# Kernel tuning notes

Measured on AMD Instinct MI355X. Metric: run time of the kernel, lower is better.

The kernel has to match this reference:

```python
import jax, jax.numpy as jnp
import numpy as np

D_MODEL = 768
NUM_HEADS = 12
DIM_QKV = D_MODEL // NUM_HEADS  # 64
NEG_INF = -1000000000.0


def setup_inputs() -> dict:
    key = jax.random.key(0)
    ks = jax.random.split(key, 12)
    B, S = 2, 2048
    def lin(kw, kb):
        # torch nn.Linear default init: U(-1/sqrt(fan_in), 1/sqrt(fan_in))
        bound = 1.0 / np.sqrt(D_MODEL)
        W = jax.random.uniform(kw, (D_MODEL, D_MODEL), jnp.float32, -bound, bound)
        b = jax.random.uniform(kb, (D_MODEL,), jnp.float32, -bound, bound)
        return W, b
    Wq, bq = lin(ks[0], ks[1])
    Wk, bk = lin(ks[2], ks[3])
    Wv, bv = lin(ks[4], ks[5])
    Wo, bo = lin(ks[6], ks[7])
    Q = jax.random.normal(ks[8], (B, S, D_MODEL), jnp.float32)
    K = jax.random.normal(ks[9], (B, S, D_MODEL), jnp.float32)
    V = jax.random.normal(ks[10], (B, S, D_MODEL), jnp.float32)
    mask = jnp.tril(jnp.ones((S, S), dtype=bool))[None, None]  # [1,1,S,S] causal
    return {"Q": Q, "K": K, "V": V, "mask": mask,
            "Wq": Wq, "bq": bq, "Wk": Wk, "bk": bk,
            "Wv": Wv, "bv": bv, "Wo": Wo, "bo": bo}


def _split_heads(x):
    B, S, _ = x.shape
    return x.reshape(B, S, NUM_HEADS, DIM_QKV).transpose(0, 2, 1, 3)  # [B,H,S,d]


def reference(Q, K, V, mask, Wq, bq, Wk, bk, Wv, bv, Wo, bo):
    # torch Linear: y = x @ W.T + b
    q = _split_heads(Q @ Wq.T + bq)
    k = _split_heads(K @ Wk.T + bk)
    v = _split_heads(V @ Wv.T + bv)
    scale = jnp.sqrt(jnp.float32(DIM_QKV))
    scores = jnp.einsum('bhqd,bhkd->bhqk', q, k) / scale  # [B,H,S,S]
    scores = jnp.where(mask, scores, NEG_INF)
    probs = jax.nn.softmax(scores, axis=-1)  # dropout p=0 -> identity
    attn = jnp.einsum('bhqk,bhkd->bhqd', probs, v)
    B, H, S, d = attn.shape
    out = attn.transpose(0, 2, 1, 3).reshape(B, S, H * d) @ Wo.T + bo
    return out, scores
```

## Files before the change

### kernel.cpp

```cpp
#include <hip/hip_runtime.h>
#include <hip/hip_bf16.h>

typedef __attribute__((ext_vector_type(8))) short short8;
typedef __attribute__((ext_vector_type(4))) short short4v;
typedef __attribute__((ext_vector_type(4))) float f32x4;

#define S_LEN 2048
#define DM 768
#define NH 12
#define HD 64
#define NB 2
#define MROWS (NB*S_LEN)
#define NEGINF (-1.0e9f)
#define XEL 3145728
#define WEL 589824

__device__ __forceinline__ unsigned short f2bf(float x) {
    __hip_bfloat16 h = __float2bfloat16(x);
    return *reinterpret_cast<unsigned short*>(&h);
}

__device__ __forceinline__ void gl_lds16(const unsigned short* g, unsigned short* l) {
    __builtin_amdgcn_global_load_lds(
        (const __attribute__((address_space(1))) unsigned int*)g,
        (__attribute__((address_space(3))) unsigned int*)l, 16, 0, 0);
}

__global__ __launch_bounds__(256) void cvt_w_kernel(
    const float* w0, const float* w1, const float* w2, const float* w3,
    unsigned short* dst)
{
    int which = blockIdx.y;
    const float* src = (which == 0) ? w0 : (which == 1) ? w1 : (which == 2) ? w2 : w3;
    size_t idx = (size_t)blockIdx.x * 256 + threadIdx.x;
    const float* s = src + idx * 8;
    f32x4 v0 = *(const f32x4*)s;
    f32x4 v1 = *(const f32x4*)(s + 4);
    short8 o;
    o[0] = (short)f2bf(v0[0]); o[1] = (short)f2bf(v0[1]);
    o[2] = (short)f2bf(v0[2]); o[3] = (short)f2bf(v0[3]);
    o[4] = (short)f2bf(v1[0]); o[5] = (short)f2bf(v1[1]);
    o[6] = (short)f2bf(v1[2]); o[7] = (short)f2bf(v1[3]);
    *(short8*)&dst[(size_t)which * WEL + idx * 8] = o;
}

__global__ __launch_bounds__(256) void gemm_qkv_kernel(
    const float* Xq, const float* Xk, const float* Xv, const unsigned short* Wall,
    const float* b0, const float* b1, const float* b2, unsigned short* qh)
{
    int by = blockIdx.y;
    const float* A = (by == 0) ? Xq : (by == 1) ? Xk : Xv;
    const unsigned short* W = Wall + (size_t)by * WEL;
    const float* bias = (by == 0) ? b0 : (by == 1) ? b1 : b2;
    int bx = blockIdx.x;
    int im = (bx & 7) + 8 * (bx / 48);
    int jn = (bx >> 3) % 6;
    int i0 = im * 128, j0 = jn * 128;

    __shared__ unsigned short As[128 * 64];
    __shared__ unsigned short Ws[128 * 64];

    int t = threadIdx.x;
    int w = t >> 6, lane = t & 63, g = lane >> 4, fr = lane & 15;
    int wm = w >> 1, wn = w & 1;

    f32x4 acc[4][4];
    for (int i = 0; i < 4; ++i)
        for (int j = 0; j < 4; ++j)
            acc[i][j] = (f32x4){0.f, 0.f, 0.f, 0.f};

    int boff = t * 16;
    int arow = t >> 3;
    int acol = (t & 7) * 8;

    for (int k0 = 0; k0 < DM; k0 += 64) {
        __syncthreads();
        for (int r = 0; r < 4; ++r) {
            int b = r * 4096 + boff;
            int row = b >> 7, colb = b & 127;
            gl_lds16(&W[(size_t)(j0 + row) * DM + k0 + (colb >> 1)],
                     (unsigned short*)((char*)Ws + b));
        }
        for (int rr = 0; rr < 4; ++rr) {
            int row = rr * 32 + arow;
            const float* src = &A[(size_t)(i0 + row) * DM + k0 + acol];
            f32x4 v0 = *(const f32x4*)src;
            f32x4 v1 = *(const f32x4*)(src + 4);
            short8 o;
            o[0] = (short)f2bf(v0[0]); o[1] = (short)f2bf(v0[1]);
            o[2] = (short)f2bf(v0[2]); o[3] = (short)f2bf(v0[3]);
            o[4] = (short)f2bf(v1[0]); o[5] = (short)f2bf(v1[1]);
            o[6] = (short)f2bf(v1[2]); o[7] = (short)f2bf(v1[3]);
            *(short8*)&As[row * 64 + acol] = o;
        }
        __syncthreads();
        for (int kk = 0; kk < 2; ++kk) {
            short8 af[4], wf[4];
            for (int it = 0; it < 4; ++it)
                af[it] = *(const short8*)&As[(wm * 64 + it * 16 + fr) * 64 + kk * 32 + g * 8];
            for (int jt = 0; jt < 4; ++jt)
                wf[jt] = *(const short8*)&Ws[(wn * 64 + jt * 16 + fr) * 64 + kk * 32 + g * 8];
            for (int it = 0; it < 4; ++it)
                for (int jt = 0; jt < 4; ++jt)
                    acc[it][jt] = __builtin_amdgcn_mfma_f32_16x16x32_bf16(af[it], wf[jt], acc[it][jt], 0, 0, 0);
        }
    }

    float scl = (by == 0) ? 0.125f : 1.0f;
    if (by < 2) {
        unsigned short* outp = qh + (size_t)by * XEL;
        for (int jt = 0; jt < 4; ++jt) {
            int j = j0 + wn * 64 + jt * 16 + fr;
            float bv = bias[j];
            int h = j >> 6, dq = j & 63;
            for (int it = 0; it < 4; ++it)
                for (int r = 0; r < 4; ++r) {
                    int i = i0 + wm * 64 + it * 16 + g * 4 + r;
                    int bb = i >> 11, s = i & 2047;
                    outp[((size_t)((bb * NH + h) * S_LEN) + s) * HD + dq] = f2bf((acc[it][jt][r] + bv) * scl);
                }
        }
    } else {
        unsigned short* vtp = qh + (size_t)2 * XEL;
        for (int jt = 0; jt < 4; ++jt) {
            int j = j0 + wn * 64 + jt * 16 + fr;
            float bv = bias[j];
            int h = j >> 6, dq = j & 63;
            for (int it = 0; it < 4; ++it) {
                int ibase = i0 + wm * 64 + it * 16 + g * 4;
                int bb = ibase >> 11, s = ibase & 2047;
                short4v o;
                for (int r = 0; r < 4; ++r) o[r] = (short)f2bf(acc[it][jt][r] + bv);
                *(short4v*)&vtp[((size_t)(bb * NH + h) * HD + dq) * S_LEN + s] = o;
            }
        }
    }
}

__global__ __launch_bounds__(256) void gemm_o_kernel(
    const unsigned short* A, const unsigned short* W, const float* bias, float* f_out)
{
    int bx = blockIdx.x;
    int im = (bx & 7) + 8 * (bx / 96);
    int jn = (bx >> 3) % 12;
    int i0 = im * 64, j0 = jn * 64;

    __shared__ unsigned short As[64 * 64];
    __shared__ unsigned short Ws[64 * 64];

    int t = threadIdx.x;
    int w = t >> 6, lane = t & 63, g = lane >> 4, fr = lane & 15;
    int wm = w >> 1, wn = w & 1;

    f32x4 acc[2][2];
    for (int i = 0; i < 2; ++i)
        for (int j = 0; j < 2; ++j)
            acc[i][j] = (f32x4){0.f, 0.f, 0.f, 0.f};

    int boff = t * 16;

    for (int k0 = 0; k0 < DM; k0 += 64) {
        __syncthreads();
        for (int r = 0; r < 2; ++r) {
            int b = r * 4096 + boff;
            int row = b >> 7, colb = b & 127;
            gl_lds16(&A[(size_t)(i0 + row) * DM + k0 + (colb >> 1)],
                     (unsigned short*)((char*)As + b));
            gl_lds16(&W[(size_t)(j0 + row) * DM + k0 + (colb >> 1)],
                     (unsigned short*)((char*)Ws + b));
        }
        __syncthreads();
        for (int kk = 0; kk < 2; ++kk) {
            short8 af[2], wf[2];
            for (int it = 0; it < 2; ++it)
                af[it] = *(const short8*)&As[(wm * 32 + it * 16 + fr) * 64 + kk * 32 + g * 8];
            for (int jt = 0; jt < 2; ++jt)
                wf[jt] = *(const short8*)&Ws[(wn * 32 + jt * 16 + fr) * 64 + kk * 32 + g * 8];
            for (int it = 0; it < 2; ++it)
                for (int jt = 0; jt < 2; ++jt)
                    acc[it][jt] = __builtin_amdgcn_mfma_f32_16x16x32_bf16(af[it], wf[jt], acc[it][jt], 0, 0, 0);
        }
    }

    for (int jt = 0; jt < 2; ++jt) {
        int j = j0 + wn * 32 + jt * 16 + fr;
        float bv = bias[j];
        for (int it = 0; it < 2; ++it)
            for (int r = 0; r < 4; ++r) {
                int i = i0 + wm * 32 + it * 16 + g * 4 + r;
                f_out[(size_t)i * DM + j] = acc[it][jt][r] + bv;
            }
    }
}

__global__ __launch_bounds__(256) void attn_kernel(
    const unsigned short* q, const unsigned short* k, const unsigned short* vt,
    float* scores, unsigned short* attn)
{
    __shared__ unsigned short KV[2][8192];
    __shared__ float P[4][16][68];
    int t = threadIdx.x;
    int w = t >> 6, lane = t & 63, g = lane >> 4, fr = lane & 15;
    float (*Pw)[68] = P[w];

    int bid = blockIdx.x;
    int bh = (bid & 7) * 3 + (bid >> 3) % 3;
    int s = bid / 24;
    int myspan = (w < 2) ? s : 63 - s;
    int qbase = myspan * 32 + (w & 1) * 16;
    int myNt = ((myspan * 32 + 31) >> 6) + 1;
    int ntmax = (((63 - s) * 32 + 31) >> 6) + 1;
    int b = bh / NH, h = bh % NH;

    const unsigned short* qp = q + (size_t)bh * S_LEN * HD;
    const unsigned short* kp = k + (size_t)bh * S_LEN * HD;
    const unsigned short* vp = vt + (size_t)bh * HD * S_LEN;
    float* sp = scores + (size_t)bh * S_LEN * S_LEN;

    int srow2 = t >> 3;
    int scb = (t & 7) * 16;
    int swzu = (fr & 7) * 8;

    short8 qf0 = *(const short8*)&qp[(size_t)(qbase + fr) * HD + g * 8];
    short8 qf1 = *(const short8*)&qp[(size_t)(qbase + fr) * HD + 32 + g * 8];

    f32x4 acc[4];
    for (int jt = 0; jt < 4; ++jt) acc[jt] = (f32x4){0.f, 0.f, 0.f, 0.f};
    float m_run = -1e30f, l_run = 0.f;

    for (int rd = 0; rd < 2; ++rd) {
        int row = rd * 32 + srow2;
        int sc = (scb ^ ((row & 7) << 4)) >> 1;
        gl_lds16(&kp[(size_t)row * HD + sc], &KV[0][(size_t)t * 8 + rd * 2048]);
        gl_lds16(&vp[(size_t)row * S_LEN + sc], &KV[0][4096 + (size_t)t * 8 + rd * 2048]);
    }

    int buf = 0;
    for (int kt = 0; kt < ntmax; ++kt) {
        __syncthreads();
        if (kt + 1 < ntmax) {
            int kb2 = (kt + 1) * 64;
            for (int rd = 0; rd < 2; ++rd) {
                int row = rd * 32 + srow2;
                int sc = (scb ^ ((row & 7) << 4)) >> 1;
                gl_lds16(&kp[(size_t)(kb2 + row) * HD + sc], &KV[buf ^ 1][(size_t)t * 8 + rd * 2048]);
                gl_lds16(&vp[(size_t)row * S_LEN + kb2 + sc], &KV[buf ^ 1][4096 + (size_t)t * 8 + rd * 2048]);
            }
        }
        if (kt < myNt) {
            const unsigned short* Kb = KV[buf];
            const unsigned short* Vb = KV[buf] + 4096;
            int kb = kt * 64;
            bool diag = (kt == myNt - 1);

            short8 kf[4][2];
            for (int ktt = 0; ktt < 4; ++ktt) {
                int base = (ktt * 16 + fr) * 64;
                kf[ktt][0] = *(const short8*)&Kb[base + ((g * 8) ^ swzu)];
                kf[ktt][1] = *(const short8*)&Kb[base + ((32 + g * 8) ^ swzu)];
            }
            __builtin_amdgcn_s_setprio(1);
            f32x4 s4v[4];
            for (int ktt = 0; ktt < 4; ++ktt) {
                f32x4 s4 = (f32x4){0.f, 0.f, 0.f, 0.f};
                s4 = __builtin_amdgcn_mfma_f32_16x16x32_bf16(qf0, kf[ktt][0], s4, 0, 0, 0);
                s4 = __builtin_amdgcn_mfma_f32_16x16x32_bf16(qf1, kf[ktt][1], s4, 0, 0, 0);
                s4v[ktt] = s4;
            }
            __builtin_amdgcn_s_setprio(0);
            if (diag) {
                for (int ktt = 0; ktt < 4; ++ktt) {
                    int kg = kb + ktt * 16 + fr;
                    for (int r = 0; r < 4; ++r) {
                        int qg = qbase + g * 4 + r;
                        float val = (kg <= qg) ? s4v[ktt][r] : NEGINF;
                        Pw[g * 4 + r][ktt * 16 + fr] = val;
                    }
                }
            } else {
                for (int ktt = 0; ktt < 4; ++ktt)
                    for (int r = 0; r < 4; ++r)
                        Pw[g * 4 + r][ktt * 16 + fr] = s4v[ktt][r];
            }
            for (int pass = 0; pass < 4; ++pass) {
                int rr = pass * 4 + g;
                int cc = fr * 4;
                f32x4 vv = *(const f32x4*)&Pw[rr][cc];
                __builtin_nontemporal_store(vv, (f32x4*)&sp[(size_t)(qbase + rr) * S_LEN + kb + cc]);
            }
            f32x4 pA = *(const f32x4*)&Pw[fr][g * 8];
            f32x4 pB = *(const f32x4*)&Pw[fr][g * 8 + 4];
            f32x4 pC = *(const f32x4*)&Pw[fr][32 + g * 8];
            f32x4 pD = *(const f32x4*)&Pw[fr][32 + g * 8 + 4];
            float pv[16];
            pv[0]=pA[0]; pv[1]=pA[1]; pv[2]=pA[2]; pv[3]=pA[3];
            pv[4]=pB[0]; pv[5]=pB[1]; pv[6]=pB[2]; pv[7]=pB[3];
            pv[8]=pC[0]; pv[9]=pC[1]; pv[10]=pC[2]; pv[11]=pC[3];
            pv[12]=pD[0]; pv[13]=pD[1]; pv[14]=pD[2]; pv[15]=pD[3];
            float tmax = pv[0];
            for (int e = 1; e < 16; ++e) tmax = fmaxf(tmax, pv[e]);
            tmax = fmaxf(tmax, __shfl_xor(tmax, 16, 64));
            tmax = fmaxf(tmax, __shfl_xor(tmax, 32, 64));
            float m_new = fmaxf(m_run, tmax);
            float corr = __expf(m_run - m_new);
            float lsum = 0.f;
            for (int e = 0; e < 16; ++e) { pv[e] = __expf(pv[e] - m_new); lsum += pv[e]; }
            lsum += __shfl_xor(lsum, 16, 64);
            lsum += __shfl_xor(lsum, 32, 64);
            l_run = l_run * corr + lsum;
            m_run = m_new;
            short8 pa0, pa1;
            for (int e = 0; e < 8; ++e) { pa0[e] = (short)f2bf(pv[e]); pa1[e] = (short)f2bf(pv[8 + e]); }
            float fc[4];
            for (int r = 0; r < 4; ++r) fc[r] = __shfl(corr, g * 4 + r, 64);
            for (int jt = 0; jt < 4; ++jt)
                for (int r = 0; r < 4; ++r) acc[jt][r] *= fc[r];
            short8 vf[4][2];
            for (int jt = 0; jt < 4; ++jt) {
                int base = (jt * 16 + fr) * 64;
                vf[jt][0] = *(const short8*)&Vb[base + ((g * 8) ^ swzu)];
                vf[jt][1] = *(const short8*)&Vb[base + ((32 + g * 8) ^ swzu)];
            }
            __builtin_amdgcn_s_setprio(1);
            for (int jt = 0; jt < 4; ++jt) {
                acc[jt] = __builtin_amdgcn_mfma_f32_16x16x32_bf16(pa0, vf[jt][0], acc[jt], 0, 0, 0);
                acc[jt] = __builtin_amdgcn_mfma_f32_16x16x32_bf16(pa1, vf[jt][1], acc[jt], 0, 0, 0);
            }
            __builtin_amdgcn_s_setprio(0);
        }
        buf ^= 1;
    }
    float linv[4];
    for (int r = 0; r < 4; ++r) linv[r] = 1.0f / __shfl(l_run, g * 4 + r, 64);
    for (int jt = 0; jt < 4; ++jt) {
        int col = h * HD + jt * 16 + fr;
        for (int r = 0; r < 4; ++r) {
            int i = b * S_LEN + qbase + g * 4 + r;
            attn[(size_t)i * DM + col] = f2bf(acc[jt][r] * linv[r]);
        }
    }
    f32x4 nv = (f32x4){NEGINF, NEGINF, NEGINF, NEGINF};
    int fill0 = myNt * 64;
    for (int rr = 0; rr < 16; ++rr) {
        float* rowp = &sp[(size_t)(qbase + rr) * S_LEN];
        for (int c = fill0 + lane * 4; c < S_LEN; c += 256)
            __builtin_nontemporal_store(nv, (f32x4*)(rowp + c));
    }
}

extern "C" void kernel_launch(void* const* d_in, const int* in_sizes, int n_in,
                              void* d_out, int out_size, void* d_ws, size_t ws_size,
                              hipStream_t stream) {
    const float* Q  = (const float*)d_in[0];
    const float* K  = (const float*)d_in[1];
    const float* V  = (const float*)d_in[2];
    const float* Wq = (const float*)d_in[4];
    const float* bq = (const float*)d_in[5];
    const float* Wk = (const float*)d_in[6];
    const float* bk = (const float*)d_in[7];
    const float* Wv = (const float*)d_in[8];
    const float* bv = (const float*)d_in[9];
    const float* Wo = (const float*)d_in[10];
    const float* bo = (const float*)d_in[11];

    float* out = (float*)d_out;
    float* scores = out + (size_t)MROWS * DM;

    unsigned short* ws   = (unsigned short*)d_ws;
    unsigned short* Wbf  = ws;
    unsigned short* qh   = Wbf + (size_t)4 * WEL;
    unsigned short* attn = qh + (size_t)3 * XEL;

    cvt_w_kernel<<<dim3(288, 4), 256, 0, stream>>>(Wq, Wk, Wv, Wo, Wbf);
    gemm_qkv_kernel<<<dim3(192, 3), 256, 0, stream>>>(Q, K, V, Wbf, bq, bk, bv, qh);
    attn_kernel<<<dim3(768), 256, 0, stream>>>(qh, qh + (size_t)XEL, qh + (size_t)2 * XEL,
                                               scores, attn);
    gemm_o_kernel<<<dim3(768), 256, 0, stream>>>(attn, Wbf + (size_t)3 * WEL, bo, out);
}
```

Baseline: 157.5 us.

## Load K/V fragments directly from global memory instead of LDS double buffer

New measurement: 175.7 us. 11.5% more time.

```diff
diff --git a/kernel.cpp b/kernel.cpp
--- a/kernel.cpp
+++ b/kernel.cpp
@@ -197,7 +197,6 @@
     const unsigned short* q, const unsigned short* k, const unsigned short* vt,
     float* scores, unsigned short* attn)
 {
-    __shared__ unsigned short KV[2][8192];
     __shared__ float P[4][16][68];
     int t = threadIdx.x;
     int w = t >> 6, lane = t & 63, g = lane >> 4, fr = lane & 15;
@@ -209,7 +208,6 @@
     int myspan = (w < 2) ? s : 63 - s;
     int qbase = myspan * 32 + (w & 1) * 16;
     int myNt = ((myspan * 32 + 31) >> 6) + 1;
-    int ntmax = (((63 - s) * 32 + 31) >> 6) + 1;
     int b = bh / NH, h = bh % NH;
 
     const unsigned short* qp = q + (size_t)bh * S_LEN * HD;
@@ -217,10 +215,6 @@
     const unsigned short* vp = vt + (size_t)bh * HD * S_LEN;
     float* sp = scores + (size_t)bh * S_LEN * S_LEN;
 
-    int srow2 = t >> 3;
-    int scb = (t & 7) * 16;
-    int swzu = (fr & 7) * 8;
-
     short8 qf0 = *(const short8*)&qp[(size_t)(qbase + fr) * HD + g * 8];
     short8 qf1 = *(const short8*)&qp[(size_t)(qbase + fr) * HD + 32 + g * 8];
 
@@ -228,107 +222,82 @@
     for (int jt = 0; jt < 4; ++jt) acc[jt] = (f32x4){0.f, 0.f, 0.f, 0.f};
     float m_run = -1e30f, l_run = 0.f;
 
-    for (int rd = 0; rd < 2; ++rd) {
-        int row = rd * 32 + srow2;
-        int sc = (scb ^ ((row & 7) << 4)) >> 1;
-        gl_lds16(&kp[(size_t)row * HD + sc], &KV[0][(size_t)t * 8 + rd * 2048]);
-        gl_lds16(&vp[(size_t)row * S_LEN + sc], &KV[0][4096 + (size_t)t * 8 + rd * 2048]);
-    }
-
-    int buf = 0;
-    for (int kt = 0; kt < ntmax; ++kt) {
-        __syncthreads();
-        if (kt + 1 < ntmax) {
-            int kb2 = (kt + 1) * 64;
-            for (int rd = 0; rd < 2; ++rd) {
-                int row = rd * 32 + srow2;
-                int sc = (scb ^ ((row & 7) << 4)) >> 1;
-                gl_lds16(&kp[(size_t)(kb2 + row) * HD + sc], &KV[buf ^ 1][(size_t)t * 8 + rd * 2048]);
-                gl_lds16(&vp[(size_t)row * S_LEN + kb2 + sc], &KV[buf ^ 1][4096 + (size_t)t * 8 + rd * 2048]);
+    for (int kt = 0; kt < myNt; ++kt) {
+        int kb = kt * 64;
+        bool diag = (kt == myNt - 1);
+
+        short8 kf[4][2];
+        for (int ktt = 0; ktt < 4; ++ktt) {
+            kf[ktt][0] = *(const short8*)&kp[(size_t)(kb + ktt * 16 + fr) * HD + g * 8];
+            kf[ktt][1] = *(const short8*)&kp[(size_t)(kb + ktt * 16 + fr) * HD + 32 + g * 8];
+        }
+        __builtin_amdgcn_s_setprio(1);
+        f32x4 s4v[4];
+        for (int ktt = 0; ktt < 4; ++ktt) {
+            f32x4 s4 = (f32x4){0.f, 0.f, 0.f, 0.f};
+            s4 = __builtin_amdgcn_mfma_f32_16x16x32_bf16(qf0, kf[ktt][0], s4, 0, 0, 0);
+            s4 = __builtin_amdgcn_mfma_f32_16x16x32_bf16(qf1, kf[ktt][1], s4, 0, 0, 0);
+            s4v[ktt] = s4;
+        }
+        __builtin_amdgcn_s_setprio(0);
+        if (diag) {
+            for (int ktt = 0; ktt < 4; ++ktt) {
+                int kg = kb + ktt * 16 + fr;
+                for (int r = 0; r < 4; ++r) {
+                    int qg = qbase + g * 4 + r;
+                    float val = (kg <= qg) ? s4v[ktt][r] : NEGINF;
+                    Pw[g * 4 + r][ktt * 16 + fr] = val;
+                }
             }
-        }
-        if (kt < myNt) {
-            const unsigned short* Kb = KV[buf];
-            const unsigned short* Vb = KV[buf] + 4096;
-            int kb = kt * 64;
-            bool diag = (kt == myNt - 1);
-
-            short8 kf[4][2];
-            for (int ktt = 0; ktt < 4; ++ktt) {
-                int base = (ktt * 16 + fr) * 64;
-                kf[ktt][0] = *(const short8*)&Kb[base + ((g * 8) ^ swzu)];
-                kf[ktt][1] = *(const short8*)&Kb[base + ((32 + g * 8) ^ swzu)];
-            }
-            __builtin_amdgcn_s_setprio(1);
-            f32x4 s4v[4];
-            for (int ktt = 0; ktt < 4; ++ktt) {
-                f32x4 s4 = (f32x4){0.f, 0.f, 0.f, 0.f};
-                s4 = __builtin_amdgcn_mfma_f32_16x16x32_bf16(qf0, kf[ktt][0], s4, 0, 0, 0);
-                s4 = __builtin_amdgcn_mfma_f32_16x16x32_bf16(qf1, kf[ktt][1], s4, 0, 0, 0);
-                s4v[ktt] = s4;
-            }
-            __builtin_amdgcn_s_setprio(0);
-            if (diag) {
-                for (int ktt = 0; ktt < 4; ++ktt) {
-                    int kg = kb + ktt * 16 + fr;
-                    for (int r = 0; r < 4; ++r) {
-                        int qg = qbase + g * 4 + r;
-                        float val = (kg <= qg) ? s4v[ktt][r] : NEGINF;
-                        Pw[g * 4 + r][ktt * 16 + fr] = val;
-                    }
-                }
-            } else {
-                for (int ktt = 0; ktt < 4; ++ktt)
-                    for (int r = 0; r < 4; ++r)
-                        Pw[g * 4 + r][ktt * 16 + fr] = s4v[ktt][r];
-            }
-            for (int pass = 0; pass < 4; ++pass) {
-                int rr = pass * 4 + g;
-                int cc = fr * 4;
-                f32x4 vv = *(const f32x4*)&Pw[rr][cc];
-                __builtin_nontemporal_store(vv, (f32x4*)&sp[(size_t)(qbase + rr) * S_LEN + kb + cc]);
-            }
-            f32x4 pA = *(const f32x4*)&Pw[fr][g * 8];
-            f32x4 pB = *(const f32x4*)&Pw[fr][g * 8 + 4];
-            f32x4 pC = *(const f32x4*)&Pw[fr][32 + g * 8];
-            f32x4 pD = *(const f32x4*)&Pw[fr][32 + g * 8 + 4];
-            float pv[16];
-            pv[0]=pA[0]; pv[1]=pA[1]; pv[2]=pA[2]; pv[3]=pA[3];
-            pv[4]=pB[0]; pv[5]=pB[1]; pv[6]=pB[2]; pv[7]=pB[3];
-            pv[8]=pC[0]; pv[9]=pC[1]; pv[10]=pC[2]; pv[11]=pC[3];
-            pv[12]=pD[0]; pv[13]=pD[1]; pv[14]=pD[2]; pv[15]=pD[3];
-            float tmax = pv[0];
-            for (int e = 1; e < 16; ++e) tmax = fmaxf(tmax, pv[e]);
-            tmax = fmaxf(tmax, __shfl_xor(tmax, 16, 64));
-            tmax = fmaxf(tmax, __shfl_xor(tmax, 32, 64));
-            float m_new = fmaxf(m_run, tmax);
-            float corr = __expf(m_run - m_new);
-            float lsum = 0.f;
-            for (int e = 0; e < 16; ++e) { pv[e] = __expf(pv[e] - m_new); lsum += pv[e]; }
-            lsum += __shfl_xor(lsum, 16, 64);
-            lsum += __shfl_xor(lsum, 32, 64);
-            l_run = l_run * corr + lsum;
-            m_run = m_new;
-            short8 pa0, pa1;
-            for (int e = 0; e < 8; ++e) { pa0[e] = (short)f2bf(pv[e]); pa1[e] = (short)f2bf(pv[8 + e]); }
-            float fc[4];
-            for (int r = 0; r < 4; ++r) fc[r] = __shfl(corr, g * 4 + r, 64);
-            for (int jt = 0; jt < 4; ++jt)
-                for (int r = 0; r < 4; ++r) acc[jt][r] *= fc[r];
-            short8 vf[4][2];
-            for (int jt = 0; jt < 4; ++jt) {
-                int base = (jt * 16 + fr) * 64;
-                vf[jt][0] = *(const short8*)&Vb[base + ((g * 8) ^ swzu)];
-                vf[jt][1] = *(const short8*)&Vb[base + ((32 + g * 8) ^ swzu)];
-            }
-            __builtin_amdgcn_s_setprio(1);
-            for (int jt = 0; jt < 4; ++jt) {
-                acc[jt] = __builtin_amdgcn_mfma_f32_16x16x32_bf16(pa0, vf[jt][0], acc[jt], 0, 0, 0);
-                acc[jt] = __builtin_amdgcn_mfma_f32_16x16x32_bf16(pa1, vf[jt][1], acc[jt], 0, 0, 0);
-            }
-            __builtin_amdgcn_s_setprio(0);
-        }
-        buf ^= 1;
+        } else {
+            for (int ktt = 0; ktt < 4; ++ktt)
+                for (int r = 0; r < 4; ++r)
+                    Pw[g * 4 + r][ktt * 16 + fr] = s4v[ktt][r];
+        }
+        for (int pass = 0; pass < 4; ++pass) {
+            int rr = pass * 4 + g;
+            int cc = fr * 4;
+            f32x4 vv = *(const f32x4*)&Pw[rr][cc];
+            __builtin_nontemporal_store(vv, (f32x4*)&sp[(size_t)(qbase + rr) * S_LEN + kb + cc]);
+        }
+        f32x4 pA = *(const f32x4*)&Pw[fr][g * 8];
+        f32x4 pB = *(const f32x4*)&Pw[fr][g * 8 + 4];
+        f32x4 pC = *(const f32x4*)&Pw[fr][32 + g * 8];
+        f32x4 pD = *(const f32x4*)&Pw[fr][32 + g * 8 + 4];
+        float pv[16];
+        pv[0]=pA[0]; pv[1]=pA[1]; pv[2]=pA[2]; pv[3]=pA[3];
+        pv[4]=pB[0]; pv[5]=pB[1]; pv[6]=pB[2]; pv[7]=pB[3];
+        pv[8]=pC[0]; pv[9]=pC[1]; pv[10]=pC[2]; pv[11]=pC[3];
+        pv[12]=pD[0]; pv[13]=pD[1]; pv[14]=pD[2]; pv[15]=pD[3];
+        float tmax = pv[0];
+        for (int e = 1; e < 16; ++e) tmax = fmaxf(tmax, pv[e]);
+        tmax = fmaxf(tmax, __shfl_xor(tmax, 16, 64));
+        tmax = fmaxf(tmax, __shfl_xor(tmax, 32, 64));
+        float m_new = fmaxf(m_run, tmax);
+        float corr = __expf(m_run - m_new);
+        float lsum = 0.f;
+        for (int e = 0; e < 16; ++e) { pv[e] = __expf(pv[e] - m_new); lsum += pv[e]; }
+        lsum += __shfl_xor(lsum, 16, 64);
+        lsum += __shfl_xor(lsum, 32, 64);
+        l_run = l_run * corr + lsum;
+        m_run = m_new;
+        short8 pa0, pa1;
+        for (int e = 0; e < 8; ++e) { pa0[e] = (short)f2bf(pv[e]); pa1[e] = (short)f2bf(pv[8 + e]); }
+        float fc[4];
+        for (int r = 0; r < 4; ++r) fc[r] = __shfl(corr, g * 4 + r, 64);
+        for (int jt = 0; jt < 4; ++jt)
+            for (int r = 0; r < 4; ++r) acc[jt][r] *= fc[r];
+        short8 vf[4][2];
+        for (int jt = 0; jt < 4; ++jt) {
+            vf[jt][0] = *(const short8*)&vp[(size_t)(jt * 16 + fr) * S_LEN + kb + g * 8];
+            vf[jt][1] = *(const short8*)&vp[(size_t)(jt * 16 + fr) * S_LEN + kb + 32 + g * 8];
+        }
+        __builtin_amdgcn_s_setprio(1);
+        for (int jt = 0; jt < 4; ++jt) {
+            acc[jt] = __builtin_amdgcn_mfma_f32_16x16x32_bf16(pa0, vf[jt][0], acc[jt], 0, 0, 0);
+            acc[jt] = __builtin_amdgcn_mfma_f32_16x16x32_bf16(pa1, vf[jt][1], acc[jt], 0, 0, 0);
+        }
+        __builtin_amdgcn_s_setprio(0);
     }
     float linv[4];
     for (int r = 0; r < 4; ++r) linv[r] = 1.0f / __shfl(l_run, g * 4 + r, 64);
```

## Fuse weight bf16 conversion into GEMMs and read V directly from global

Applied to the files above, without the earlier changes.

After: 181.2 us. 1.15x slower.

```diff
diff --git a/kernel.cpp b/kernel.cpp
--- a/kernel.cpp
+++ b/kernel.cpp
@@ -26,31 +26,14 @@
         (__attribute__((address_space(3))) unsigned int*)l, 16, 0, 0);
 }
 
-__global__ __launch_bounds__(256) void cvt_w_kernel(
-    const float* w0, const float* w1, const float* w2, const float* w3,
-    unsigned short* dst)
-{
-    int which = blockIdx.y;
-    const float* src = (which == 0) ? w0 : (which == 1) ? w1 : (which == 2) ? w2 : w3;
-    size_t idx = (size_t)blockIdx.x * 256 + threadIdx.x;
-    const float* s = src + idx * 8;
-    f32x4 v0 = *(const f32x4*)s;
-    f32x4 v1 = *(const f32x4*)(s + 4);
-    short8 o;
-    o[0] = (short)f2bf(v0[0]); o[1] = (short)f2bf(v0[1]);
-    o[2] = (short)f2bf(v0[2]); o[3] = (short)f2bf(v0[3]);
-    o[4] = (short)f2bf(v1[0]); o[5] = (short)f2bf(v1[1]);
-    o[6] = (short)f2bf(v1[2]); o[7] = (short)f2bf(v1[3]);
-    *(short8*)&dst[(size_t)which * WEL + idx * 8] = o;
-}
-
 __global__ __launch_bounds__(256) void gemm_qkv_kernel(
-    const float* Xq, const float* Xk, const float* Xv, const unsigned short* Wall,
+    const float* Xq, const float* Xk, const float* Xv,
+    const float* W0, const float* W1, const float* W2,
     const float* b0, const float* b1, const float* b2, unsigned short* qh)
 {
     int by = blockIdx.y;
     const float* A = (by == 0) ? Xq : (by == 1) ? Xk : Xv;
-    const unsigned short* W = Wall + (size_t)by * WEL;
+    const float* W = (by == 0) ? W0 : (by == 1) ? W1 : W2;
     const float* bias = (by == 0) ? b0 : (by == 1) ? b1 : b2;
     int bx = blockIdx.x;
     int im = (bx & 7) + 8 * (bx / 48);
@@ -69,29 +52,31 @@
         for (int j = 0; j < 4; ++j)
             acc[i][j] = (f32x4){0.f, 0.f, 0.f, 0.f};
 
-    int boff = t * 16;
     int arow = t >> 3;
     int acol = (t & 7) * 8;
 
     for (int k0 = 0; k0 < DM; k0 += 64) {
         __syncthreads();
-        for (int r = 0; r < 4; ++r) {
-            int b = r * 4096 + boff;
-            int row = b >> 7, colb = b & 127;
-            gl_lds16(&W[(size_t)(j0 + row) * DM + k0 + (colb >> 1)],
-                     (unsigned short*)((char*)Ws + b));
-        }
         for (int rr = 0; rr < 4; ++rr) {
             int row = rr * 32 + arow;
-            const float* src = &A[(size_t)(i0 + row) * DM + k0 + acol];
-            f32x4 v0 = *(const f32x4*)src;
-            f32x4 v1 = *(const f32x4*)(src + 4);
+            const float* srca = &A[(size_t)(i0 + row) * DM + k0 + acol];
+            f32x4 v0 = *(const f32x4*)srca;
+            f32x4 v1 = *(const f32x4*)(srca + 4);
             short8 o;
             o[0] = (short)f2bf(v0[0]); o[1] = (short)f2bf(v0[1]);
             o[2] = (short)f2bf(v0[2]); o[3] = (short)f2bf(v0[3]);
             o[4] = (short)f2bf(v1[0]); o[5] = (short)f2bf(v1[1]);
             o[6] = (short)f2bf(v1[2]); o[7] = (short)f2bf(v1[3]);
             *(short8*)&As[row * 64 + acol] = o;
+            const float* srcw = &W[(size_t)(j0 + row) * DM + k0 + acol];
+            f32x4 w0v = *(const f32x4*)srcw;
+            f32x4 w1v = *(const f32x4*)(srcw + 4);
+            short8 ow;
+            ow[0] = (short)f2bf(w0v[0]); ow[1] = (short)f2bf(w0v[1]);
+            ow[2] = (short)f2bf(w0v[2]); ow[3] = (short)f2bf(w0v[3]);
+            ow[4] = (short)f2bf(w1v[0]); ow[5] = (short)f2bf(w1v[1]);
+            ow[6] = (short)f2bf(w1v[2]); ow[7] = (short)f2bf(w1v[3]);
+            *(short8*)&Ws[row * 64 + acol] = ow;
         }
         __syncthreads();
         for (int kk = 0; kk < 2; ++kk) {
@@ -138,7 +123,7 @@
 }
 
 __global__ __launch_bounds__(256) void gemm_o_kernel(
-    const unsigned short* A, const unsigned short* W, const float* bias, float* f_out)
+    const unsigned short* A, const float* W, const float* bias, float* f_out)
 {
     int bx = blockIdx.x;
     int im = (bx & 7) + 8 * (bx / 96);
@@ -158,6 +143,7 @@
             acc[i][j] = (f32x4){0.f, 0.f, 0.f, 0.f};
 
     int boff = t * 16;
+    int arow = t >> 3, acol = (t & 7) * 8;
 
     for (int k0 = 0; k0 < DM; k0 += 64) {
         __syncthreads();
@@ -166,8 +152,18 @@
             int row = b >> 7, colb = b & 127;
             gl_lds16(&A[(size_t)(i0 + row) * DM + k0 + (colb >> 1)],
                      (unsigned short*)((char*)As + b));
-            gl_lds16(&W[(size_t)(j0 + row) * DM + k0 + (colb >> 1)],
-                     (unsigned short*)((char*)Ws + b));
+        }
+        for (int rr = 0; rr < 2; ++rr) {
+            int row = rr * 32 + arow;
+            const float* srcw = &W[(size_t)(j0 + row) * DM + k0 + acol];
+            f32x4 w0v = *(const f32x4*)srcw;
+            f32x4 w1v = *(const f32x4*)(srcw + 4);
+            short8 ow;
+            ow[0] = (short)f2bf(w0v[0]); ow[1] = (short)f2bf(w0v[1]);
+            ow[2] = (short)f2bf(w0v[2]); ow[3] = (short)f2bf(w0v[3]);
+            ow[4] = (short)f2bf(w1v[0]); ow[5] = (short)f2bf(w1v[1]);
+            ow[6] = (short)f2bf(w1v[2]); ow[7] = (short)f2bf(w1v[3]);
+            *(short8*)&Ws[row * 64 + acol] = ow;
         }
         __syncthreads();
         for (int kk = 0; kk < 2; ++kk) {
@@ -193,11 +189,11 @@
     }
 }
 
-__global__ __launch_bounds__(256) void attn_kernel(
+__global__ __launch_bounds__(256, 4) void attn_kernel(
     const unsigned short* q, const unsigned short* k, const unsigned short* vt,
     float* scores, unsigned short* attn)
 {
-    __shared__ unsigned short KV[2][8192];
+    __shared__ unsigned short Ks[2][4096];
     __shared__ float P[4][16][68];
     int t = threadIdx.x;
     int w = t >> 6, lane = t & 63, g = lane >> 4, fr = lane & 15;
@@ -231,8 +227,7 @@
     for (int rd = 0; rd < 2; ++rd) {
         int row = rd * 32 + srow2;
         int sc = (scb ^ ((row & 7) << 4)) >> 1;
-        gl_lds16(&kp[(size_t)row * HD + sc], &KV[0][(size_t)t * 8 + rd * 2048]);
-        gl_lds16(&vp[(size_t)row * S_LEN + sc], &KV[0][4096 + (size_t)t * 8 + rd * 2048]);
+        gl_lds16(&kp[(size_t)row * HD + sc], &Ks[0][(size_t)t * 8 + rd * 2048]);
     }
 
     int buf = 0;
@@ -243,13 +238,11 @@
             for (int rd = 0; rd < 2; ++rd) {
                 int row = rd * 32 + srow2;
                 int sc = (scb ^ ((row & 7) << 4)) >> 1;
-                gl_lds16(&kp[(size_t)(kb2 + row) * HD + sc], &KV[buf ^ 1][(size_t)t * 8 + rd * 2048]);
-                gl_lds16(&vp[(size_t)row * S_LEN + kb2 + sc], &KV[buf ^ 1][4096 + (size_t)t * 8 + rd * 2048]);
+                gl_lds16(&kp[(size_t)(kb2 + row) * HD + sc], &Ks[buf ^ 1][(size_t)t * 8 + rd * 2048]);
             }
         }
         if (kt < myNt) {
-            const unsigned short* Kb = KV[buf];
-            const unsigned short* Vb = KV[buf] + 4096;
+            const unsigned short* Kb = Ks[buf];
             int kb = kt * 64;
             bool diag = (kt == myNt - 1);
 
@@ -317,9 +310,8 @@
                 for (int r = 0; r < 4; ++r) acc[jt][r] *= fc[r];
             short8 vf[4][2];
             for (int jt = 0; jt < 4; ++jt) {
-                int base = (jt * 16 + fr) * 64;
-                vf[jt][0] = *(const short8*)&Vb[base + ((g * 8) ^ swzu)];
-                vf[jt][1] = *(const short8*)&Vb[base + ((32 + g * 8) ^ swzu)];
+                vf[jt][0] = *(const short8*)&vp[(size_t)(jt * 16 + fr) * S_LEN + kb + g * 8];
+                vf[jt][1] = *(const short8*)&vp[(size_t)(jt * 16 + fr) * S_LEN + kb + 32 + g * 8];
             }
             __builtin_amdgcn_s_setprio(1);
             for (int jt = 0; jt < 4; ++jt) {
@@ -366,14 +358,12 @@
     float* out = (float*)d_out;
     float* scores = out + (size_t)MROWS * DM;
 
-    unsigned short* ws   = (unsigned short*)d_ws;
-    unsigned short* Wbf  = ws;
-    unsigned short* qh   = Wbf + (size_t)4 * WEL;
-    unsigned short* attn = qh + (size_t)3 * XEL;
-
-    cvt_w_kernel<<<dim3(288, 4), 256, 0, stream>>>(Wq, Wk, Wv, Wo, Wbf);
-    gemm_qkv_kernel<<<dim3(192, 3), 256, 0, stream>>>(Q, K, V, Wbf, bq, bk, bv, qh);
+    unsigned short* ws    = (unsigned short*)d_ws;
+    unsigned short* qh    = ws;
+    unsigned short* attnb = qh + (size_t)3 * XEL;
+
+    gemm_qkv_kernel<<<dim3(192, 3), 256, 0, stream>>>(Q, K, V, Wq, Wk, Wv, bq, bk, bv, qh);
     attn_kernel<<<dim3(768), 256, 0, stream>>>(qh, qh + (size_t)XEL, qh + (size_t)2 * XEL,
-                                               scores, attn);
-    gemm_o_kernel<<<dim3(768), 256, 0, stream>>>(attn, Wbf + (size_t)3 * WEL, bo, out);
-}
+                                               scores, attnb);
+    gemm_o_kernel<<<dim3(768), 256, 0, stream>>>(attnb, Wo, bo, out);
+}
```
